# Performance work log

Measured on AMD Instinct MI355X. Metric: run time of the kernel, lower is better.

The kernel has to match this reference:

```python
import jax, jax.numpy as jnp
import numpy as np

N_GENE = 4264
IN_DIM = 1613
N_REL = 5
DIM1, DIM2, DIM3 = 1340, 920, 740
N_DRUG = 20000
N_EDGE = 100000
N_TOTAL = N_DRUG + N_GENE  # nodes after concatenating gene_emb


def setup_inputs() -> dict:
    key = jax.random.key(0)
    ks = jax.random.split(key, 16)
    s = 0.02  # weight init scale for numerical stability
    return {
        "x": jax.random.normal(ks[0], (N_DRUG, IN_DIM), jnp.float32),
        "edge_index": jax.random.randint(ks[1], (2, N_EDGE), 0, N_TOTAL),
        "edge_type": jax.random.randint(ks[2], (N_EDGE,), 0, N_REL),
        "gene_emb": jax.random.normal(ks[3], (N_GENE, IN_DIM), jnp.float32),
        "W1": jax.random.normal(ks[4], (N_REL, IN_DIM, DIM1), jnp.float32) * s,
        "root1": jax.random.normal(ks[5], (IN_DIM, DIM1), jnp.float32) * s,
        "b1": jnp.zeros((DIM1,), jnp.float32),
        "W2": jax.random.normal(ks[6], (N_REL, DIM1, DIM2), jnp.float32) * s,
        "root2": jax.random.normal(ks[7], (DIM1, DIM2), jnp.float32) * s,
        "b2": jnp.zeros((DIM2,), jnp.float32),
        "lin1_w": jax.random.normal(ks[8], (DIM2, DIM3), jnp.float32) * s,
        "lin1_b": jnp.zeros((DIM3,), jnp.float32),
        "lin2_w": jax.random.normal(ks[9], (DIM3, 2), jnp.float32) * s,
        "lin2_b": jnp.zeros((2,), jnp.float32),
    }


def rgcn_layer(h, W, root, b, src, dst, etype):
    """PyG RGCNConv (aggr='mean'): out_i = root^T h_i + b + sum_r mean_{j in N_r(i)} W_r^T h_j."""
    out = h @ root + b  # [N, out_dim] root transform
    for r in range(N_REL):  # small fixed relation loop
        mask = (etype == r)
        # per-relation transform at node granularity, then edge gather
        msg = jnp.where(mask[:, None], (h @ W[r])[src], 0.0)  # [E, out_dim]
        agg = jax.ops.segment_sum(msg, dst, num_segments=N_TOTAL)
        cnt = jax.ops.segment_sum(mask.astype(h.dtype), dst, num_segments=N_TOTAL)
        out = out + agg / jnp.maximum(cnt, 1.0)[:, None]
    return out


def reference(x, edge_index, edge_type, gene_emb, W1, root1, b1, W2, root2, b2,
              lin1_w, lin1_b, lin2_w, lin2_b):
    src, dst = edge_index[0], edge_index[1]
    h = jnp.concatenate([x, gene_emb], axis=0)  # [N_TOTAL, IN_DIM]
    h = jax.nn.relu(rgcn_layer(h, W1, root1, b1, src, dst, edge_type))
    h = jax.nn.relu(rgcn_layer(h, W2, root2, b2, src, dst, edge_type))
    h = jax.nn.relu(h @ lin1_w + lin1_b)
    emb = h  # dropout is identity in eval mode
    logits = h @ lin2_w + lin2_b
    return jax.nn.log_softmax(logits, axis=-1), emb
```

## Files before the change

### kernel.cpp

```cpp
#include <hip/hip_runtime.h>

#define NT 24264
#define MT 24320
#define NDRUG 20000
#define NGENE 4264
#define NE 100000
#define NREL 5
#define IND 1613
#define D1 1340
#define D2 920
#define D3 740
#define PIN 1632
#define PD1 1344
#define PD2 928
#define ND1 1408
#define ND2 1024
#define ND3 768

typedef unsigned short u16;
typedef unsigned int u32;
typedef short bf16x8 __attribute__((ext_vector_type(8)));
typedef float f32x4 __attribute__((ext_vector_type(4)));

__device__ __forceinline__ u16 f2bf(float f) {
  u32 u = __builtin_bit_cast(u32, f);
  u32 r = (u + 0x7FFFu + ((u >> 16) & 1u)) >> 16;
  return (u16)r;
}
__device__ __forceinline__ float bf2f(u16 h) {
  u32 u = ((u32)h) << 16;
  return __builtin_bit_cast(float, u);
}
__device__ __forceinline__ int iclamp(int v, int lo, int hi) {
  return v < lo ? lo : (v > hi ? hi : v);
}

__device__ __forceinline__ void gload_lds16(const u16* g, u16* l) {
  __builtin_amdgcn_global_load_lds(
      (const __attribute__((address_space(1))) unsigned int*)(const void*)g,
      (__attribute__((address_space(3))) unsigned int*)(void*)l,
      16, 0, 0);
}

__global__ __launch_bounds__(256) void zero_i32_k(int* __restrict__ p, int n) {
  int i = blockIdx.x * 256 + threadIdx.x;
  if (i < n) p[i] = 0;
}

__global__ __launch_bounds__(256) void transpose_k(
    const float* __restrict__ in, u16* __restrict__ out,
    int K, int N, int ldo, size_t in_batch, size_t out_batch)
{
  __shared__ u16 tile[32][33];
  const int b = blockIdx.z;
  in  += (size_t)b * in_batch;
  out += (size_t)b * out_batch;
  const int n0 = blockIdx.x * 32, k0 = blockIdx.y * 32;
  const int tx = threadIdx.x, ty = threadIdx.y;
  for (int i = ty; i < 32; i += 8) {
    int k = k0 + i, n = n0 + tx;
    tile[i][tx] = (k < K && n < N) ? f2bf(in[(size_t)k * N + n]) : (u16)0;
  }
  __syncthreads();
  for (int i = ty; i < 32; i += 8) {
    int n = n0 + i, k = k0 + tx;
    if (n < N && k < K) out[(size_t)n * ldo + k] = tile[tx][i];
  }
}

__global__ __launch_bounds__(256) void build_h0_k(
    const float* __restrict__ x, const float* __restrict__ gene, u16* __restrict__ h0)
{
  const int row = blockIdx.x;
  const float* s = (row < NDRUG) ? (x + (size_t)row * IND)
                                 : (gene + (size_t)(row - NDRUG) * IND);
  u16* d = h0 + (size_t)row * PIN;
  for (int i = threadIdx.x; i < PIN; i += 256) d[i] = (i < IND) ? f2bf(s[i]) : (u16)0;
}

__global__ __launch_bounds__(256) void count_k(
    const int* __restrict__ dst, const int* __restrict__ et, int* __restrict__ cnt)
{
  int e = blockIdx.x * 256 + threadIdx.x;
  if (e < NE) {
    int r = iclamp(et[e], 0, NREL - 1);
    int d = iclamp(dst[e], 0, NT - 1);
    atomicAdd(&cnt[(size_t)r * NT + d], 1);
  }
}

__global__ __launch_bounds__(256) void scan_simple_k(
    const int* __restrict__ in, int* __restrict__ out, int n)
{
  __shared__ int part[256];
  const int tid = threadIdx.x;
  const int chunk = (n + 255) / 256;
  const int lo = tid * chunk;
  const int hi = (lo + chunk < n) ? (lo + chunk) : n;
  int s = 0;
  for (int i = lo; i < hi; ++i) s += in[i];
  part[tid] = s;
  __syncthreads();
  if (tid == 0) {
    int run = 0;
    for (int i = 0; i < 256; ++i) { int t = part[i]; part[i] = run; run += t; }
  }
  __syncthreads();
  int run = part[tid];
  for (int i = lo; i < hi; ++i) { out[i] = run; run += in[i]; }
}

__global__ __launch_bounds__(256) void fill_k(
    const int* __restrict__ src, const int* __restrict__ dst, const int* __restrict__ et,
    const int* __restrict__ offs, int* __restrict__ pos, int* __restrict__ esrc)
{
  int e = blockIdx.x * 256 + threadIdx.x;
  if (e < NE) {
    int r = iclamp(et[e], 0, NREL - 1);
    int d = iclamp(dst[e], 0, NT - 1);
    int b = r * NT + d;
    int p = offs[b] + atomicAdd(&pos[b], 1);
    p = iclamp(p, 0, NE - 1);
    esrc[p] = iclamp(src[e], 0, NT - 1);
  }
}

__global__ __launch_bounds__(256) void gather_k(
    const int* __restrict__ esrc, const int* __restrict__ offs, const int* __restrict__ cnt,
    int rel, const u16* __restrict__ H, int ldh, int nvec, u16* __restrict__ out, int ldo)
{
  const int i = blockIdx.x;
  const int b = rel * NT + i;
  int n = iclamp(cnt[b], 0, NE);
  int o = iclamp(offs[b], 0, NE - 1);
  if (o + n > NE) n = NE - o;
  u16* op = out + (size_t)i * ldo;
  if (n <= 0) {
    uint4 z = {0, 0, 0, 0};
    for (int v = threadIdx.x; v < nvec; v += 256) *(uint4*)(op + v * 8) = z;
    return;
  }
  const float inv = 1.0f / (float)n;
  for (int v = threadIdx.x; v < nvec; v += 256) {
    float acc[8] = {};
    for (int e = 0; e < n; ++e) {
      int si = iclamp(esrc[o + e], 0, NT - 1);
      const u16* hp = H + (size_t)si * ldh + v * 8;
      uint4 xv = *(const uint4*)hp;
      const u16* xu = (const u16*)&xv;
      #pragma unroll
      for (int j = 0; j < 8; ++j) acc[j] += bf2f(xu[j]);
    }
    u16 r[8];
    #pragma unroll
    for (int j = 0; j < 8; ++j) {
      float f = acc[j] * inv;
      f = (f == f) ? f : 0.0f;
      r[j] = f2bf(f);
    }
    *(uint4*)(op + v * 8) = *(uint4*)r;
  }
}

template <int MODE, typename CT>
__global__ __launch_bounds__(256, 2) void gemm_nt(
    const u16* __restrict__ A, int lda,
    const u16* __restrict__ BT, int ldb,
    CT* __restrict__ C, int ldc,
    int M, int N, int K,
    const float* __restrict__ bias)
{
  constexpr int BM = 128, BN = 128, BK = 32;
  __shared__ u16 As[BM * BK];
  __shared__ u16 Bs[BN * BK];
  const int tid = threadIdx.x;
  const int lane = tid & 63;
  const int wid = tid >> 6;
  const int wm = wid >> 1, wn = wid & 1;
  const int q = lane >> 4, l15 = lane & 15;
  const int m0 = blockIdx.y * BM, n0 = blockIdx.x * BN;

  const int srow = wid * 16 + (lane >> 2);
  const int skk  = (lane & 3) * 8;
  const u16* gA0 = A  + (size_t)(m0 + srow) * lda + skk;
  const u16* gA1 = A  + (size_t)(m0 + 64 + srow) * lda + skk;
  const u16* gB0 = BT + (size_t)(n0 + srow) * ldb + skk;
  const u16* gB1 = BT + (size_t)(n0 + 64 + srow) * ldb + skk;
  u16* lA0 = &As[(size_t)(wid * 16) * BK];
  u16* lA1 = &As[(size_t)(64 + wid * 16) * BK];
  u16* lB0 = &Bs[(size_t)(wid * 16) * BK];
  u16* lB1 = &Bs[(size_t)(64 + wid * 16) * BK];

  f32x4 acc[4][4] = {};

  const int ktiles = K / BK;
  for (int kt = 0; kt < ktiles; ++kt) {
    gload_lds16(gA0, lA0);
    gload_lds16(gA1, lA1);
    gload_lds16(gB0, lB0);
    gload_lds16(gB1, lB1);
    gA0 += BK; gA1 += BK; gB0 += BK; gB1 += BK;
    __syncthreads();

    bf16x8 af[4], bfr[4];
    #pragma unroll
    for (int i = 0; i < 4; ++i)
      af[i] = *(const bf16x8*)&As[(wm * 64 + i * 16 + l15) * BK + q * 8];
    #pragma unroll
    for (int j = 0; j < 4; ++j)
      bfr[j] = *(const bf16x8*)&Bs[(wn * 64 + j * 16 + l15) * BK + q * 8];
    #pragma unroll
    for (int i = 0; i < 4; ++i)
      #pragma unroll
      for (int j = 0; j < 4; ++j)
        acc[i][j] = __builtin_amdgcn_mfma_f32_16x16x32_bf16(af[i], bfr[j], acc[i][j], 0, 0, 0);
    __syncthreads();
  }

  #pragma unroll
  for (int i = 0; i < 4; ++i) {
    #pragma unroll
    for (int t = 0; t < 4; ++t) {
      const int r = m0 + wm * 64 + i * 16 + q * 4 + t;
      if (r >= M) continue;
      #pragma unroll
      for (int j = 0; j < 4; ++j) {
        const int c = n0 + wn * 64 + j * 16 + l15;
        if (c < N) {
          const size_t idx = (size_t)r * ldc + c;
          float v = acc[i][j][t];
          v = (v == v) ? v : 0.0f;
          if (MODE == 0) {
            C[idx] = (CT)f2bf(v + bias[c]);
          } else if (MODE == 1) {
            float c0 = bf2f((u16)C[idx]);
            c0 = (c0 == c0) ? c0 : 0.0f;
            C[idx] = (CT)f2bf(c0 + v);
          } else {
            float s = v + bias[c];
            s = (s > 0.0f) ? s : 0.0f;
            ((float*)C)[idx] = s;
          }
        }
      }
    }
  }
}

__global__ __launch_bounds__(256) void relu_pad_k(u16* __restrict__ h, int real, int pad)
{
  const int r = blockIdx.x;
  u16* p = h + (size_t)r * pad;
  for (int c = threadIdx.x; c < pad; c += 256) {
    u16 x = p[c];
    p[c] = (c < real && bf2f(x) > 0.0f) ? x : (u16)0;
  }
}

__global__ __launch_bounds__(256) void head_k(
    const float* __restrict__ emb,
    const float* __restrict__ w, const float* __restrict__ b, float* __restrict__ out)
{
  const int row = blockIdx.x * 4 + (threadIdx.x >> 6);
  const int lane = threadIdx.x & 63;
  if (row >= NT) return;
  const float* e = emb + (size_t)row * D3;
  float s0 = 0.f, s1 = 0.f;
  for (int k = lane; k < D3; k += 64) {
    float v = e[k];
    s0 += v * w[2 * k];
    s1 += v * w[2 * k + 1];
  }
  #pragma unroll
  for (int off = 32; off > 0; off >>= 1) {
    s0 += __shfl_down(s0, off, 64);
    s1 += __shfl_down(s1, off, 64);
  }
  if (lane == 0) {
    s0 += b[0]; s1 += b[1];
    s0 = (s0 == s0) ? s0 : 0.0f;
    s1 = (s1 == s1) ? s1 : 0.0f;
    float m = fmaxf(s0, s1);
    float lse = m + logf(expf(s0 - m) + expf(s1 - m));
    out[2 * (size_t)row]     = s0 - lse;
    out[2 * (size_t)row + 1] = s1 - lse;
  }
}

extern "C" void kernel_launch(void* const* d_in, const int* in_sizes, int n_in,
                              void* d_out, int out_size, void* d_ws, size_t ws_size,
                              hipStream_t stream)
{
  (void)in_sizes; (void)n_in; (void)out_size;
  const float* x     = (const float*)d_in[0];
  const int*   ei    = (const int*)d_in[1];
  const int*   et    = (const int*)d_in[2];
  const float* gene  = (const float*)d_in[3];
  const float* W1    = (const float*)d_in[4];
  const float* root1 = (const float*)d_in[5];
  const float* b1    = (const float*)d_in[6];
  const float* W2    = (const float*)d_in[7];
  const float* root2 = (const float*)d_in[8];
  const float* b2    = (const float*)d_in[9];
  const float* l1w   = (const float*)d_in[10];
  const float* l1b   = (const float*)d_in[11];
  const float* l2w   = (const float*)d_in[12];
  const float* l2b   = (const float*)d_in[13];
  const int* srcI = ei;
  const int* dstI = ei + NE;

  char* base = (char*)d_ws;
  size_t off = 0;
  auto take = [&](size_t bytes) -> char* {
    char* p = base + off;
    off += (bytes + 255) & ~(size_t)255;
    return p;
  };
  u16* regA = (u16*)take((size_t)MT * PIN * 2);
  u16* regB = (u16*)take((size_t)MT * PIN * 2);
  u16* regC = (u16*)take((size_t)MT * PD1 * 2);
  int* cnt  = (int*)take((size_t)NREL * NT * 4);
  int* pos  = (int*)take((size_t)NREL * NT * 4);
  int* offs = (int*)take((size_t)NREL * NT * 4);
  int* esrc = (int*)take((size_t)NE * 4);
  u16* BTr1 = (u16*)take((size_t)ND1 * PIN * 2);
  u16* BTW1 = (u16*)take((size_t)NREL * ND1 * PIN * 2);
  u16* BTr2 = (u16*)take((size_t)ND2 * PD1 * 2);
  u16* BTW2 = (u16*)take((size_t)NREL * ND2 * PD1 * 2);
  u16* BTl1 = (u16*)take((size_t)ND3 * PD2 * 2);
  char* wzend = base + off;

  if (off > ws_size) return;

  float* outp = (float*)d_out;
  float* emb  = outp + (size_t)NT * 2;

  zero_i32_k<<<(NREL * NT + 255) / 256, 256, 0, stream>>>(cnt, NREL * NT);
  zero_i32_k<<<(NREL * NT + 255) / 256, 256, 0, stream>>>(pos, NREL * NT);
  count_k<<<(NE + 255) / 256, 256, 0, stream>>>(dstI, et, cnt);
  scan_simple_k<<<1, 256, 0, stream>>>(cnt, offs, NREL * NT);
  fill_k<<<(NE + 255) / 256, 256, 0, stream>>>(srcI, dstI, et, offs, pos, esrc);

  {
    size_t wzn = (size_t)(wzend - (char*)BTr1) / 4;
    zero_i32_k<<<(int)((wzn + 255) / 256), 256, 0, stream>>>((int*)BTr1, (int)wzn);
  }

  dim3 tb(32, 8);
  transpose_k<<<dim3((D1 + 31) / 32, (IND + 31) / 32, 1),    tb, 0, stream>>>(root1, BTr1, IND, D1, PIN, 0, 0);
  transpose_k<<<dim3((D1 + 31) / 32, (IND + 31) / 32, NREL), tb, 0, stream>>>(W1, BTW1, IND, D1, PIN, (size_t)IND * D1, (size_t)ND1 * PIN);
  transpose_k<<<dim3((D2 + 31) / 32, (D1 + 31) / 32, 1),     tb, 0, stream>>>(root2, BTr2, D1, D2, PD1, 0, 0);
  transpose_k<<<dim3((D2 + 31) / 32, (D1 + 31) / 32, NREL),  tb, 0, stream>>>(W2, BTW2, D1, D2, PD1, (size_t)D1 * D2, (size_t)ND2 * PD1);
  transpose_k<<<dim3((D3 + 31) / 32, (D2 + 31) / 32, 1),     tb, 0, stream>>>(l1w, BTl1, D2, D3, PD2, 0, 0);

  build_h0_k<<<NT, 256, 0, stream>>>(x, gene, regA);

  dim3 g1((D1 + 127) / 128, (NT + 127) / 128);
  gemm_nt<0, u16><<<g1, 256, 0, stream>>>(regA, PIN, BTr1, PIN, regC, PD1, NT, D1, PIN, b1);
  for (int r = 0; r < NREL; ++r) {
    gather_k<<<NT, 256, 0, stream>>>(esrc, offs, cnt, r, regA, PIN, PIN / 8, regB, PIN);
    gemm_nt<1, u16><<<g1, 256, 0, stream>>>(regB, PIN, BTW1 + (size_t)r * ND1 * PIN, PIN, regC, PD1, NT, D1, PIN, nullptr);
  }
  relu_pad_k<<<NT, 256, 0, stream>>>(regC, D1, PD1);

  dim3 g2((D2 + 127) / 128, (NT + 127) / 128);
  gemm_nt<0, u16><<<g2, 256, 0, stream>>>(regC, PD1, BTr2, PD1, regA, PD2, NT, D2, PD1, b2);
  for (int r = 0; r < NREL; ++r) {
    gather_k<<<NT, 256, 0, stream>>>(esrc, offs, cnt, r, regC, PD1, PD1 / 8, regB, PD1);
    gemm_nt<1, u16><<<g2, 256, 0, stream>>>(regB, PD1, BTW2 + (size_t)r * ND2 * PD1, PD1, regA, PD2, NT, D2, PD1, nullptr);
  }
  relu_pad_k<<<NT, 256, 0, stream>>>(regA, D2, PD2);

  dim3 g3((D3 + 127) / 128, (NT + 127) / 128);
  gemm_nt<2, float><<<g3, 256, 0, stream>>>(regA, PD2, BTl1, PD2, emb, D3, NT, D3, PD2, l1b);

  head_k<<<(NT + 3) / 4, 256, 0, stream>>>(emb, l2w, l2b, outp);
}
```

Before: 3.058 ms.

## Fuse root and per-relation GEMMs into one concatenated-K GEMM with XCD swizzle

Result: faster. 2.756 ms (-9.9%).

```diff
diff --git a/kernel.cpp b/kernel.cpp
--- a/kernel.cpp
+++ b/kernel.cpp
@@ -13,6 +13,8 @@
 #define PIN 1632
 #define PD1 1344
 #define PD2 928
+#define CAT1 (6 * PIN)
+#define CAT2 (6 * PD1)
 #define ND1 1408
 #define ND2 1024
 #define ND3 768
@@ -42,9 +44,28 @@
       16, 0, 0);
 }
 
+__device__ __forceinline__ void swz_tile(int& m0, int& n0) {
+  const int gx = gridDim.x;
+  const int nwg = gx * gridDim.y;
+  const int orig = blockIdx.y * gx + blockIdx.x;
+  const int q = nwg >> 3, rr = nwg & 7;
+  const int xcd = orig & 7, idx = orig >> 3;
+  const int nid = (xcd < rr ? xcd * (q + 1) : rr * (q + 1) + (xcd - rr) * q) + idx;
+  m0 = (nid / gx) * 128;
+  n0 = (nid % gx) * 128;
+}
+
 __global__ __launch_bounds__(256) void zero_i32_k(int* __restrict__ p, int n) {
   int i = blockIdx.x * 256 + threadIdx.x;
   if (i < n) p[i] = 0;
+}
+
+__global__ __launch_bounds__(256) void zero_pad_cols_k(u16* __restrict__ h, int D, int P, int rows) {
+  int r = blockIdx.x * 256 + threadIdx.x;
+  if (r < rows) {
+    u16* p = h + (size_t)r * P;
+    for (int c = D; c < P; ++c) p[c] = 0;
+  }
 }
 
 __global__ __launch_bounds__(256) void transpose_k(
@@ -178,7 +199,8 @@
   const int wid = tid >> 6;
   const int wm = wid >> 1, wn = wid & 1;
   const int q = lane >> 4, l15 = lane & 15;
-  const int m0 = blockIdx.y * BM, n0 = blockIdx.x * BN;
+  int m0, n0;
+  swz_tile(m0, n0);
 
   const int srow = wid * 16 + (lane >> 2);
   const int skk  = (lane & 3) * 8;
@@ -247,6 +269,88 @@
   }
 }
 
+__global__ __launch_bounds__(256, 2) void gemm_cat(
+    const u16* __restrict__ A0, int lda0, int K0,
+    const u16* __restrict__ A1, int lda1,
+    const u16* __restrict__ BT, int ldb,
+    u16* __restrict__ C, int ldc,
+    int M, int N, int Ktot,
+    const float* __restrict__ bias)
+{
+  constexpr int BM = 128, BN = 128, BK = 32;
+  __shared__ u16 As[BM * BK];
+  __shared__ u16 Bs[BN * BK];
+  const int tid = threadIdx.x;
+  const int lane = tid & 63;
+  const int wid = tid >> 6;
+  const int wm = wid >> 1, wn = wid & 1;
+  const int q = lane >> 4, l15 = lane & 15;
+  int m0, n0;
+  swz_tile(m0, n0);
+
+  const int srow = wid * 16 + (lane >> 2);
+  const int skk  = (lane & 3) * 8;
+  const u16* a0lo = A0 + (size_t)(m0 + srow) * lda0 + skk;
+  const u16* a0hi = A0 + (size_t)(m0 + 64 + srow) * lda0 + skk;
+  const u16* a1lo = A1 + (size_t)(m0 + srow) * lda1 + skk;
+  const u16* a1hi = A1 + (size_t)(m0 + 64 + srow) * lda1 + skk;
+  const u16* b0   = BT + (size_t)(n0 + srow) * ldb + skk;
+  const u16* b1p  = BT + (size_t)(n0 + 64 + srow) * ldb + skk;
+  u16* lA0 = &As[(size_t)(wid * 16) * BK];
+  u16* lA1 = &As[(size_t)(64 + wid * 16) * BK];
+  u16* lB0 = &Bs[(size_t)(wid * 16) * BK];
+  u16* lB1 = &Bs[(size_t)(64 + wid * 16) * BK];
+
+  f32x4 acc[4][4] = {};
+
+  const int ktiles = Ktot / BK;
+  for (int kt = 0; kt < ktiles; ++kt) {
+    const int k0 = kt * BK;
+    const u16 *ga0, *ga1;
+    if (k0 < K0) { ga0 = a0lo + k0; ga1 = a0hi + k0; }
+    else         { ga0 = a1lo + (k0 - K0); ga1 = a1hi + (k0 - K0); }
+    gload_lds16(ga0, lA0);
+    gload_lds16(ga1, lA1);
+    gload_lds16(b0 + k0, lB0);
+    gload_lds16(b1p + k0, lB1);
+    __syncthreads();
+
+    bf16x8 af[4], bfr[4];
+    #pragma unroll
+    for (int i = 0; i < 4; ++i)
+      af[i] = *(const bf16x8*)&As[(wm * 64 + i * 16 + l15) * BK + q * 8];
+    #pragma unroll
+    for (int j = 0; j < 4; ++j)
+      bfr[j] = *(const bf16x8*)&Bs[(wn * 64 + j * 16 + l15) * BK + q * 8];
+    #pragma unroll
+    for (int i = 0; i < 4; ++i)
+      #pragma unroll
+      for (int j = 0; j < 4; ++j)
+        acc[i][j] = __builtin_amdgcn_mfma_f32_16x16x32_bf16(af[i], bfr[j], acc[i][j], 0, 0, 0);
+    __syncthreads();
+  }
+
+  #pragma unroll
+  for (int i = 0; i < 4; ++i) {
+    #pragma unroll
+    for (int t = 0; t < 4; ++t) {
+      const int r = m0 + wm * 64 + i * 16 + q * 4 + t;
+      if (r >= M) continue;
+      #pragma unroll
+      for (int j = 0; j < 4; ++j) {
+        const int c = n0 + wn * 64 + j * 16 + l15;
+        if (c < N) {
+          float v = acc[i][j][t];
+          v = (v == v) ? v : 0.0f;
+          float s = v + bias[c];
+          s = (s > 0.0f) ? s : 0.0f;
+          C[(size_t)r * ldc + c] = f2bf(s);
+        }
+      }
+    }
+  }
+}
+
 __global__ __launch_bounds__(256) void relu_pad_k(u16* __restrict__ h, int real, int pad)
 {
   const int r = blockIdx.x;
@@ -317,20 +421,22 @@
     return p;
   };
   u16* regA = (u16*)take((size_t)MT * PIN * 2);
-  u16* regB = (u16*)take((size_t)MT * PIN * 2);
   u16* regC = (u16*)take((size_t)MT * PD1 * 2);
   int* cnt  = (int*)take((size_t)NREL * NT * 4);
   int* pos  = (int*)take((size_t)NREL * NT * 4);
   int* offs = (int*)take((size_t)NREL * NT * 4);
   int* esrc = (int*)take((size_t)NE * 4);
-  u16* BTr1 = (u16*)take((size_t)ND1 * PIN * 2);
-  u16* BTW1 = (u16*)take((size_t)NREL * ND1 * PIN * 2);
-  u16* BTr2 = (u16*)take((size_t)ND2 * PD1 * 2);
-  u16* BTW2 = (u16*)take((size_t)NREL * ND2 * PD1 * 2);
-  u16* BTl1 = (u16*)take((size_t)ND3 * PD2 * 2);
-  char* wzend = base + off;
-
-  if (off > ws_size) return;
+  char* wz0 = base + off;
+  u16* BTcat1 = (u16*)take((size_t)ND1 * CAT1 * 2);
+  u16* BTcat2 = (u16*)take((size_t)ND2 * CAT2 * 2);
+  u16* BTl1   = (u16*)take((size_t)ND3 * PD2 * 2);
+  char* wz1 = base + off;
+  const size_t base_off = off;
+  u16* bufX = (u16*)(base + base_off);
+  const size_t cat_bytes  = (size_t)MT * 5 * PIN * 2;
+  const size_t regb_bytes = (size_t)MT * PIN * 2;
+  const bool fused = (base_off + cat_bytes) <= ws_size;
+  if (!fused && (base_off + regb_bytes) > ws_size) return;
 
   float* outp = (float*)d_out;
   float* emb  = outp + (size_t)NT * 2;
@@ -342,36 +448,50 @@
   fill_k<<<(NE + 255) / 256, 256, 0, stream>>>(srcI, dstI, et, offs, pos, esrc);
 
   {
-    size_t wzn = (size_t)(wzend - (char*)BTr1) / 4;
-    zero_i32_k<<<(int)((wzn + 255) / 256), 256, 0, stream>>>((int*)BTr1, (int)wzn);
+    size_t wzn = (size_t)(wz1 - wz0) / 4;
+    zero_i32_k<<<(int)((wzn + 255) / 256), 256, 0, stream>>>((int*)wz0, (int)wzn);
   }
 
   dim3 tb(32, 8);
-  transpose_k<<<dim3((D1 + 31) / 32, (IND + 31) / 32, 1),    tb, 0, stream>>>(root1, BTr1, IND, D1, PIN, 0, 0);
-  transpose_k<<<dim3((D1 + 31) / 32, (IND + 31) / 32, NREL), tb, 0, stream>>>(W1, BTW1, IND, D1, PIN, (size_t)IND * D1, (size_t)ND1 * PIN);
-  transpose_k<<<dim3((D2 + 31) / 32, (D1 + 31) / 32, 1),     tb, 0, stream>>>(root2, BTr2, D1, D2, PD1, 0, 0);
-  transpose_k<<<dim3((D2 + 31) / 32, (D1 + 31) / 32, NREL),  tb, 0, stream>>>(W2, BTW2, D1, D2, PD1, (size_t)D1 * D2, (size_t)ND2 * PD1);
+  transpose_k<<<dim3((D1 + 31) / 32, (IND + 31) / 32, 1),    tb, 0, stream>>>(root1, BTcat1, IND, D1, CAT1, 0, 0);
+  transpose_k<<<dim3((D1 + 31) / 32, (IND + 31) / 32, NREL), tb, 0, stream>>>(W1, BTcat1 + PIN, IND, D1, CAT1, (size_t)IND * D1, (size_t)PIN);
+  transpose_k<<<dim3((D2 + 31) / 32, (D1 + 31) / 32, 1),     tb, 0, stream>>>(root2, BTcat2, D1, D2, CAT2, 0, 0);
+  transpose_k<<<dim3((D2 + 31) / 32, (D1 + 31) / 32, NREL),  tb, 0, stream>>>(W2, BTcat2 + PD1, D1, D2, CAT2, (size_t)D1 * D2, (size_t)PD1);
   transpose_k<<<dim3((D3 + 31) / 32, (D2 + 31) / 32, 1),     tb, 0, stream>>>(l1w, BTl1, D2, D3, PD2, 0, 0);
 
   build_h0_k<<<NT, 256, 0, stream>>>(x, gene, regA);
 
-  dim3 g1((D1 + 127) / 128, (NT + 127) / 128);
-  gemm_nt<0, u16><<<g1, 256, 0, stream>>>(regA, PIN, BTr1, PIN, regC, PD1, NT, D1, PIN, b1);
-  for (int r = 0; r < NREL; ++r) {
-    gather_k<<<NT, 256, 0, stream>>>(esrc, offs, cnt, r, regA, PIN, PIN / 8, regB, PIN);
-    gemm_nt<1, u16><<<g1, 256, 0, stream>>>(regB, PIN, BTW1 + (size_t)r * ND1 * PIN, PIN, regC, PD1, NT, D1, PIN, nullptr);
-  }
-  relu_pad_k<<<NT, 256, 0, stream>>>(regC, D1, PD1);
-
-  dim3 g2((D2 + 127) / 128, (NT + 127) / 128);
-  gemm_nt<0, u16><<<g2, 256, 0, stream>>>(regC, PD1, BTr2, PD1, regA, PD2, NT, D2, PD1, b2);
-  for (int r = 0; r < NREL; ++r) {
-    gather_k<<<NT, 256, 0, stream>>>(esrc, offs, cnt, r, regC, PD1, PD1 / 8, regB, PD1);
-    gemm_nt<1, u16><<<g2, 256, 0, stream>>>(regB, PD1, BTW2 + (size_t)r * ND2 * PD1, PD1, regA, PD2, NT, D2, PD1, nullptr);
-  }
-  relu_pad_k<<<NT, 256, 0, stream>>>(regA, D2, PD2);
-
-  dim3 g3((D3 + 127) / 128, (NT + 127) / 128);
+  dim3 g1((D1 + 127) / 128, (MT + 127) / 128);
+  dim3 g2((D2 + 127) / 128, (MT + 127) / 128);
+  dim3 g3((D3 + 127) / 128, (MT + 127) / 128);
+
+  if (fused) {
+    for (int r = 0; r < NREL; ++r)
+      gather_k<<<NT, 256, 0, stream>>>(esrc, offs, cnt, r, regA, PIN, PIN / 8, bufX + (size_t)r * PIN, 5 * PIN);
+    gemm_cat<<<g1, 256, 0, stream>>>(regA, PIN, PIN, bufX, 5 * PIN, BTcat1, CAT1, regC, PD1, NT, D1, CAT1, b1);
+    zero_pad_cols_k<<<(NT + 255) / 256, 256, 0, stream>>>(regC, D1, PD1, NT);
+
+    for (int r = 0; r < NREL; ++r)
+      gather_k<<<NT, 256, 0, stream>>>(esrc, offs, cnt, r, regC, PD1, PD1 / 8, bufX + (size_t)r * PD1, 5 * PD1);
+    gemm_cat<<<g2, 256, 0, stream>>>(regC, PD1, PD1, bufX, 5 * PD1, BTcat2, CAT2, regA, PD2, NT, D2, CAT2, b2);
+    zero_pad_cols_k<<<(NT + 255) / 256, 256, 0, stream>>>(regA, D2, PD2, NT);
+  } else {
+    u16* regB = bufX;
+    gemm_nt<0, u16><<<g1, 256, 0, stream>>>(regA, PIN, BTcat1, CAT1, regC, PD1, NT, D1, PIN, b1);
+    for (int r = 0; r < NREL; ++r) {
+      gather_k<<<NT, 256, 0, stream>>>(esrc, offs, cnt, r, regA, PIN, PIN / 8, regB, PIN);
+      gemm_nt<1, u16><<<g1, 256, 0, stream>>>(regB, PIN, BTcat1 + (size_t)(r + 1) * PIN, CAT1, regC, PD1, NT, D1, PIN, nullptr);
+    }
+    relu_pad_k<<<NT, 256, 0, stream>>>(regC, D1, PD1);
+
+    gemm_nt<0, u16><<<g2, 256, 0, stream>>>(regC, PD1, BTcat2, CAT2, regA, PD2, NT, D2, PD1, b2);
+    for (int r = 0; r < NREL; ++r) {
+      gather_k<<<NT, 256, 0, stream>>>(esrc, offs, cnt, r, regC, PD1, PD1 / 8, regB, PD1);
+      gemm_nt<1, u16><<<g2, 256, 0, stream>>>(regB, PD1, BTcat2 + (size_t)(r + 1) * PD1, CAT2, regA, PD2, NT, D2, PD1, nullptr);
+    }
+    relu_pad_k<<<NT, 256, 0, stream>>>(regA, D2, PD2);
+  }
+
   gemm_nt<2, float><<<g3, 256, 0, stream>>>(regA, PD2, BTl1, PD2, emb, D3, NT, D3, PD2, l1b);
 
   head_k<<<(NT + 3) / 4, 256, 0, stream>>>(emb, l2w, l2b, outp);
```

## Concatenate root and relation weights along K into one fused RGCN GEMM

Applied to the files above, without the earlier changes.

Measured after the change: 2.622 ms. -14.3%, faster.

```diff
diff --git a/kernel.cpp b/kernel.cpp
--- a/kernel.cpp
+++ b/kernel.cpp
@@ -13,6 +13,8 @@
 #define PIN 1632
 #define PD1 1344
 #define PD2 928
+#define CAT1 (6 * PIN)
+#define CAT2 (6 * PD1)
 #define ND1 1408
 #define ND2 1024
 #define ND3 768
@@ -42,9 +44,28 @@
       16, 0, 0);
 }
 
+__device__ __forceinline__ void swz_tile(int& m0, int& n0) {
+  const int gx = gridDim.x;
+  const int nwg = gx * gridDim.y;
+  const int orig = blockIdx.y * gx + blockIdx.x;
+  const int q = nwg >> 3, rr = nwg & 7;
+  const int xcd = orig & 7, idx = orig >> 3;
+  const int nid = (xcd < rr ? xcd * (q + 1) : rr * (q + 1) + (xcd - rr) * q) + idx;
+  m0 = (nid / gx) * 128;
+  n0 = (nid % gx) * 128;
+}
+
 __global__ __launch_bounds__(256) void zero_i32_k(int* __restrict__ p, int n) {
   int i = blockIdx.x * 256 + threadIdx.x;
   if (i < n) p[i] = 0;
+}
+
+__global__ __launch_bounds__(256) void zero_pad_cols_k(u16* __restrict__ h, int D, int P, int rows) {
+  int r = blockIdx.x * 256 + threadIdx.x;
+  if (r < rows) {
+    u16* p = h + (size_t)r * P;
+    for (int c = D; c < P; ++c) p[c] = 0;
+  }
 }
 
 __global__ __launch_bounds__(256) void transpose_k(
@@ -162,61 +183,74 @@
   }
 }
 
-template <int MODE, typename CT>
-__global__ __launch_bounds__(256, 2) void gemm_nt(
-    const u16* __restrict__ A, int lda,
+template <int OUTK>
+__global__ __launch_bounds__(256, 2) void gemm_rg(
+    const u16* __restrict__ A0, int lda0, int K0,
+    const u16* __restrict__ A1, int lda1, int K1,
     const u16* __restrict__ BT, int ldb,
-    CT* __restrict__ C, int ldc,
-    int M, int N, int K,
-    const float* __restrict__ bias)
+    void* __restrict__ Cv, int ldc,
+    int M, int N,
+    const float* __restrict__ bias, int acc, int relu)
 {
   constexpr int BM = 128, BN = 128, BK = 32;
-  __shared__ u16 As[BM * BK];
-  __shared__ u16 Bs[BN * BK];
+  __shared__ u16 As[2][BM * BK];
+  __shared__ u16 Bs[2][BN * BK];
   const int tid = threadIdx.x;
   const int lane = tid & 63;
   const int wid = tid >> 6;
   const int wm = wid >> 1, wn = wid & 1;
   const int q = lane >> 4, l15 = lane & 15;
-  const int m0 = blockIdx.y * BM, n0 = blockIdx.x * BN;
+  int m0, n0;
+  swz_tile(m0, n0);
 
   const int srow = wid * 16 + (lane >> 2);
   const int skk  = (lane & 3) * 8;
-  const u16* gA0 = A  + (size_t)(m0 + srow) * lda + skk;
-  const u16* gA1 = A  + (size_t)(m0 + 64 + srow) * lda + skk;
-  const u16* gB0 = BT + (size_t)(n0 + srow) * ldb + skk;
-  const u16* gB1 = BT + (size_t)(n0 + 64 + srow) * ldb + skk;
-  u16* lA0 = &As[(size_t)(wid * 16) * BK];
-  u16* lA1 = &As[(size_t)(64 + wid * 16) * BK];
-  u16* lB0 = &Bs[(size_t)(wid * 16) * BK];
-  u16* lB1 = &Bs[(size_t)(64 + wid * 16) * BK];
-
-  f32x4 acc[4][4] = {};
-
-  const int ktiles = K / BK;
+
+  auto stage = [&](int buf, int kt) {
+    const int k0 = kt * BK;
+    const u16 *glo, *ghi;
+    if (k0 < K0) {
+      glo = A0 + (size_t)(m0 + srow) * lda0 + (k0 + skk);
+      ghi = A0 + (size_t)(m0 + 64 + srow) * lda0 + (k0 + skk);
+    } else {
+      const int kk = k0 - K0;
+      glo = A1 + (size_t)(m0 + srow) * lda1 + (kk + skk);
+      ghi = A1 + (size_t)(m0 + 64 + srow) * lda1 + (kk + skk);
+    }
+    gload_lds16(glo, &As[buf][(wid * 16) * BK]);
+    gload_lds16(ghi, &As[buf][(64 + wid * 16) * BK]);
+    gload_lds16(BT + (size_t)(n0 + srow) * ldb + (k0 + skk), &Bs[buf][(wid * 16) * BK]);
+    gload_lds16(BT + (size_t)(n0 + 64 + srow) * ldb + (k0 + skk), &Bs[buf][(64 + wid * 16) * BK]);
+  };
+
+  f32x4 accf[4][4] = {};
+
+  const int ktiles = (K0 + K1) / BK;
+  stage(0, 0);
+  __syncthreads();
+  int cur = 0;
   for (int kt = 0; kt < ktiles; ++kt) {
-    gload_lds16(gA0, lA0);
-    gload_lds16(gA1, lA1);
-    gload_lds16(gB0, lB0);
-    gload_lds16(gB1, lB1);
-    gA0 += BK; gA1 += BK; gB0 += BK; gB1 += BK;
-    __syncthreads();
+    if (kt + 1 < ktiles) stage(cur ^ 1, kt + 1);
 
     bf16x8 af[4], bfr[4];
     #pragma unroll
     for (int i = 0; i < 4; ++i)
-      af[i] = *(const bf16x8*)&As[(wm * 64 + i * 16 + l15) * BK + q * 8];
+      af[i] = *(const bf16x8*)&As[cur][(wm * 64 + i * 16 + l15) * BK + q * 8];
     #pragma unroll
     for (int j = 0; j < 4; ++j)
-      bfr[j] = *(const bf16x8*)&Bs[(wn * 64 + j * 16 + l15) * BK + q * 8];
+      bfr[j] = *(const bf16x8*)&Bs[cur][(wn * 64 + j * 16 + l15) * BK + q * 8];
     #pragma unroll
     for (int i = 0; i < 4; ++i)
       #pragma unroll
       for (int j = 0; j < 4; ++j)
-        acc[i][j] = __builtin_amdgcn_mfma_f32_16x16x32_bf16(af[i], bfr[j], acc[i][j], 0, 0, 0);
+        accf[i][j] = __builtin_amdgcn_mfma_f32_16x16x32_bf16(af[i], bfr[j], accf[i][j], 0, 0, 0);
+
     __syncthreads();
-  }
-
+    cur ^= 1;
+  }
+
+  u16* Cb = (u16*)Cv;
+  float* Cf = (float*)Cv;
   #pragma unroll
   for (int i = 0; i < 4; ++i) {
     #pragma unroll
@@ -226,34 +260,26 @@
       #pragma unroll
       for (int j = 0; j < 4; ++j) {
         const int c = n0 + wn * 64 + j * 16 + l15;
-        if (c < N) {
-          const size_t idx = (size_t)r * ldc + c;
-          float v = acc[i][j][t];
-          v = (v == v) ? v : 0.0f;
-          if (MODE == 0) {
-            C[idx] = (CT)f2bf(v + bias[c]);
-          } else if (MODE == 1) {
-            float c0 = bf2f((u16)C[idx]);
+        if (c >= N) continue;
+        const size_t idx = (size_t)r * ldc + c;
+        float v = accf[i][j][t];
+        v = (v == v) ? v : 0.0f;
+        if (OUTK == 1) {
+          float s = v + bias[c];
+          s = (s > 0.0f) ? s : 0.0f;
+          Cf[idx] = s;
+        } else {
+          if (bias) v += bias[c];
+          if (acc) {
+            float c0 = bf2f(Cb[idx]);
             c0 = (c0 == c0) ? c0 : 0.0f;
-            C[idx] = (CT)f2bf(c0 + v);
-          } else {
-            float s = v + bias[c];
-            s = (s > 0.0f) ? s : 0.0f;
-            ((float*)C)[idx] = s;
+            v += c0;
           }
+          if (relu) v = (v > 0.0f) ? v : 0.0f;
+          Cb[idx] = f2bf(v);
         }
       }
     }
-  }
-}
-
-__global__ __launch_bounds__(256) void relu_pad_k(u16* __restrict__ h, int real, int pad)
-{
-  const int r = blockIdx.x;
-  u16* p = h + (size_t)r * pad;
-  for (int c = threadIdx.x; c < pad; c += 256) {
-    u16 x = p[c];
-    p[c] = (c < real && bf2f(x) > 0.0f) ? x : (u16)0;
   }
 }
 
@@ -317,20 +343,24 @@
     return p;
   };
   u16* regA = (u16*)take((size_t)MT * PIN * 2);
-  u16* regB = (u16*)take((size_t)MT * PIN * 2);
   u16* regC = (u16*)take((size_t)MT * PD1 * 2);
   int* cnt  = (int*)take((size_t)NREL * NT * 4);
   int* pos  = (int*)take((size_t)NREL * NT * 4);
   int* offs = (int*)take((size_t)NREL * NT * 4);
   int* esrc = (int*)take((size_t)NE * 4);
-  u16* BTr1 = (u16*)take((size_t)ND1 * PIN * 2);
-  u16* BTW1 = (u16*)take((size_t)NREL * ND1 * PIN * 2);
-  u16* BTr2 = (u16*)take((size_t)ND2 * PD1 * 2);
-  u16* BTW2 = (u16*)take((size_t)NREL * ND2 * PD1 * 2);
-  u16* BTl1 = (u16*)take((size_t)ND3 * PD2 * 2);
-  char* wzend = base + off;
-
-  if (off > ws_size) return;
+  char* wz0 = base + off;
+  u16* BTcat1 = (u16*)take((size_t)ND1 * CAT1 * 2);
+  u16* BTcat2 = (u16*)take((size_t)ND2 * CAT2 * 2);
+  u16* BTl1   = (u16*)take((size_t)ND3 * PD2 * 2);
+  char* wz1 = base + off;
+  const size_t base_off = off;
+
+  const size_t slot_b = (size_t)MT * PIN * 2;
+  int S = 0;
+  if (ws_size > base_off) S = (int)((ws_size - base_off) / slot_b);
+  if (S < 1) return;
+  if (S > NREL) S = NREL;
+  u16* bufX = (u16*)(base + base_off);
 
   float* outp = (float*)d_out;
   float* emb  = outp + (size_t)NT * 2;
@@ -342,37 +372,59 @@
   fill_k<<<(NE + 255) / 256, 256, 0, stream>>>(srcI, dstI, et, offs, pos, esrc);
 
   {
-    size_t wzn = (size_t)(wzend - (char*)BTr1) / 4;
-    zero_i32_k<<<(int)((wzn + 255) / 256), 256, 0, stream>>>((int*)BTr1, (int)wzn);
+    size_t wzn = (size_t)(wz1 - wz0) / 4;
+    zero_i32_k<<<(int)((wzn + 255) / 256), 256, 0, stream>>>((int*)wz0, (int)wzn);
   }
 
   dim3 tb(32, 8);
-  transpose_k<<<dim3((D1 + 31) / 32, (IND + 31) / 32, 1),    tb, 0, stream>>>(root1, BTr1, IND, D1, PIN, 0, 0);
-  transpose_k<<<dim3((D1 + 31) / 32, (IND + 31) / 32, NREL), tb, 0, stream>>>(W1, BTW1, IND, D1, PIN, (size_t)IND * D1, (size_t)ND1 * PIN);
-  transpose_k<<<dim3((D2 + 31) / 32, (D1 + 31) / 32, 1),     tb, 0, stream>>>(root2, BTr2, D1, D2, PD1, 0, 0);
-  transpose_k<<<dim3((D2 + 31) / 32, (D1 + 31) / 32, NREL),  tb, 0, stream>>>(W2, BTW2, D1, D2, PD1, (size_t)D1 * D2, (size_t)ND2 * PD1);
+  transpose_k<<<dim3((D1 + 31) / 32, (IND + 31) / 32, 1),    tb, 0, stream>>>(root1, BTcat1, IND, D1, CAT1, 0, 0);
+  transpose_k<<<dim3((D1 + 31) / 32, (IND + 31) / 32, NREL), tb, 0, stream>>>(W1, BTcat1 + PIN, IND, D1, CAT1, (size_t)IND * D1, (size_t)PIN);
+  transpose_k<<<dim3((D2 + 31) / 32, (D1 + 31) / 32, 1),     tb, 0, stream>>>(root2, BTcat2, D1, D2, CAT2, 0, 0);
+  transpose_k<<<dim3((D2 + 31) / 32, (D1 + 31) / 32, NREL),  tb, 0, stream>>>(W2, BTcat2 + PD1, D1, D2, CAT2, (size_t)D1 * D2, (size_t)PD1);
   transpose_k<<<dim3((D3 + 31) / 32, (D2 + 31) / 32, 1),     tb, 0, stream>>>(l1w, BTl1, D2, D3, PD2, 0, 0);
 
   build_h0_k<<<NT, 256, 0, stream>>>(x, gene, regA);
 
-  dim3 g1((D1 + 127) / 128, (NT + 127) / 128);
-  gemm_nt<0, u16><<<g1, 256, 0, stream>>>(regA, PIN, BTr1, PIN, regC, PD1, NT, D1, PIN, b1);
-  for (int r = 0; r < NREL; ++r) {
-    gather_k<<<NT, 256, 0, stream>>>(esrc, offs, cnt, r, regA, PIN, PIN / 8, regB, PIN);
-    gemm_nt<1, u16><<<g1, 256, 0, stream>>>(regB, PIN, BTW1 + (size_t)r * ND1 * PIN, PIN, regC, PD1, NT, D1, PIN, nullptr);
-  }
-  relu_pad_k<<<NT, 256, 0, stream>>>(regC, D1, PD1);
-
-  dim3 g2((D2 + 127) / 128, (NT + 127) / 128);
-  gemm_nt<0, u16><<<g2, 256, 0, stream>>>(regC, PD1, BTr2, PD1, regA, PD2, NT, D2, PD1, b2);
-  for (int r = 0; r < NREL; ++r) {
-    gather_k<<<NT, 256, 0, stream>>>(esrc, offs, cnt, r, regC, PD1, PD1 / 8, regB, PD1);
-    gemm_nt<1, u16><<<g2, 256, 0, stream>>>(regB, PD1, BTW2 + (size_t)r * ND2 * PD1, PD1, regA, PD2, NT, D2, PD1, nullptr);
-  }
-  relu_pad_k<<<NT, 256, 0, stream>>>(regA, D2, PD2);
-
-  dim3 g3((D3 + 127) / 128, (NT + 127) / 128);
-  gemm_nt<2, float><<<g3, 256, 0, stream>>>(regA, PD2, BTl1, PD2, emb, D3, NT, D3, PD2, l1b);
+  dim3 g1((D1 + 127) / 128, (MT + 127) / 128);
+  dim3 g2((D2 + 127) / 128, (MT + 127) / 128);
+  dim3 g3((D3 + 127) / 128, (MT + 127) / 128);
+
+  {
+    int done = 0; bool first = true;
+    while (done < NREL) {
+      const int nc = (NREL - done < S) ? (NREL - done) : S;
+      for (int j = 0; j < nc; ++j)
+        gather_k<<<NT, 256, 0, stream>>>(esrc, offs, cnt, done + j, regA, PIN, PIN / 8,
+                                         bufX + (size_t)j * PIN, nc * PIN);
+      const u16* Bp = BTcat1 + (size_t)(first ? 0 : (1 + done)) * PIN;
+      gemm_rg<0><<<g1, 256, 0, stream>>>(
+          first ? regA : nullptr, PIN, first ? PIN : 0,
+          bufX, nc * PIN, nc * PIN, Bp, CAT1, regC, PD1, NT, D1,
+          first ? b1 : nullptr, first ? 0 : 1, (done + nc == NREL) ? 1 : 0);
+      first = false; done += nc;
+    }
+    zero_pad_cols_k<<<(NT + 255) / 256, 256, 0, stream>>>(regC, D1, PD1, NT);
+  }
+
+  {
+    int done = 0; bool first = true;
+    while (done < NREL) {
+      const int nc = (NREL - done < S) ? (NREL - done) : S;
+      for (int j = 0; j < nc; ++j)
+        gather_k<<<NT, 256, 0, stream>>>(esrc, offs, cnt, done + j, regC, PD1, PD1 / 8,
+                                         bufX + (size_t)j * PD1, nc * PD1);
+      const u16* Bp = BTcat2 + (size_t)(first ? 0 : (1 + done)) * PD1;
+      gemm_rg<0><<<g2, 256, 0, stream>>>(
+          first ? regC : nullptr, PD1, first ? PD1 : 0,
+          bufX, nc * PD1, nc * PD1, Bp, CAT2, regA, PD2, NT, D2,
+          first ? b2 : nullptr, first ? 0 : 1, (done + nc == NREL) ? 1 : 0);
+      first = false; done += nc;
+    }
+    zero_pad_cols_k<<<(NT + 255) / 256, 256, 0, stream>>>(regA, D2, PD2, NT);
+  }
+
+  gemm_rg<1><<<g3, 256, 0, stream>>>(regA, PD2, PD2, nullptr, 0, 0,
+                                     BTl1, PD2, emb, D3, NT, D3, l1b, 0, 1);
 
   head_k<<<(NT + 3) / 4, 256, 0, stream>>>(emb, l2w, l2b, outp);
 }
```
